# Kernel optimization log

Hardware: AMD Instinct MI355X
Metric: run time of the kernel (lower is better)

The kernel has to match this reference:

```python
import jax, jax.numpy as jnp
import numpy as np

N_NODES = 50000
N_EDGES = 800000
IN_DIM = 128
HEADS1, D1 = 4, 16   # hidden_dim // 4 = 16, concat -> 64
HID = HEADS1 * D1    # 64
OUT_DIM = 40
NEG_SLOPE = 0.2      # PyG GATConv default


def setup_inputs() -> dict:
    key = jax.random.key(0)
    ks = jax.random.split(key, 11)
    x = jax.random.normal(ks[0], (N_NODES, IN_DIM), dtype=jnp.float32)
    edge_index = jax.random.randint(ks[1], (2, N_EDGES), 0, N_NODES)
    s1 = 1.0 / np.sqrt(IN_DIM)
    s2 = 1.0 / np.sqrt(HID)
    return {
        "x": x,
        "edge_index": edge_index,
        "W1": jax.random.normal(ks[2], (IN_DIM, HEADS1 * D1), dtype=jnp.float32) * s1,
        "a_src1": jax.random.normal(ks[3], (HEADS1, D1), dtype=jnp.float32) * s2,
        "a_dst1": jax.random.normal(ks[4], (HEADS1, D1), dtype=jnp.float32) * s2,
        "b1": jnp.zeros((HID,), dtype=jnp.float32),
        "W2": jax.random.normal(ks[5], (HID, OUT_DIM), dtype=jnp.float32) * s2,
        "a_src2": jax.random.normal(ks[6], (1, OUT_DIM), dtype=jnp.float32) * s2,
        "a_dst2": jax.random.normal(ks[7], (1, OUT_DIM), dtype=jnp.float32) * s2,
        "b2": jnp.zeros((OUT_DIM,), dtype=jnp.float32),
    }


def gat_conv(x, src, dst, W, a_src, a_dst, b, heads, d, n_nodes):
    # linear projection, split into heads: [N, H, d]
    h = (x @ W).reshape(n_nodes, heads, d)
    # per-node attention logits: [N, H]
    alpha_src = jnp.einsum("nhd,hd->nh", h, a_src)
    alpha_dst = jnp.einsum("nhd,hd->nh", h, a_dst)
    # edge attention coefficients
    e = jax.nn.leaky_relu(alpha_src[src] + alpha_dst[dst], NEG_SLOPE)  # [E, H]
    # segment softmax over incoming edges of each destination node
    e_max = jax.ops.segment_max(e, dst, num_segments=n_nodes)
    e_max = jnp.where(jnp.isfinite(e_max), e_max, 0.0)
    e_exp = jnp.exp(e - e_max[dst])
    denom = jax.ops.segment_sum(e_exp, dst, num_segments=n_nodes)
    alpha = e_exp / (denom[dst] + 1e-16)  # [E, H]
    # weighted scatter-aggregate of source messages
    out = jax.ops.segment_sum(h[src] * alpha[..., None], dst, num_segments=n_nodes)
    return out.reshape(n_nodes, heads * d) + b


def reference(x, edge_index, W1, a_src1, a_dst1, b1, W2, a_src2, a_dst2, b2):
    n = x.shape[0]
    # PyG GATConv add_self_loops=True
    loop = jnp.arange(n, dtype=edge_index.dtype)
    src = jnp.concatenate([edge_index[0], loop])
    dst = jnp.concatenate([edge_index[1], loop])
    h = jax.nn.relu(gat_conv(x, src, dst, W1, a_src1, a_dst1, b1, HEADS1, D1, n))
    # dropout is identity in eval mode
    h = gat_conv(h, src, dst, W2, a_src2, a_dst2, b2, 1, OUT_DIM, n)
    return jax.nn.log_softmax(h, axis=1)
```

## Files before the change

### kernel.cpp

```cpp
#include <hip/hip_runtime.h>
#include <hip/hip_fp16.h>
#include <math.h>

#define NN    50000
#define NE0   800000
#define NE    850000
#define INDIM 128
#define HID   64
#define OUTD  40

#define NB    391
#define BSH   7
#define BCAP  3072

typedef unsigned short u16;
typedef unsigned char  u8;

__device__ inline u16 f2bf(float f) {
    unsigned u = __float_as_uint(f);
    return (u16)((u + 0x8000u) >> 16);
}
__device__ inline float bf2f(u16 h) {
    return __uint_as_float((unsigned)h << 16);
}

__global__ __launch_bounds__(512) void k_binit(int* __restrict__ bcur) {
    int i = threadIdx.x;
    if (i < NB) bcur[i] = i * BCAP;
}

__global__ __launch_bounds__(256) void k_bin(const int* __restrict__ ei,
                                             int* __restrict__ bcur,
                                             unsigned int* __restrict__ epack) {
    __shared__ int lh[NB];
    __shared__ int lbase[NB];
    __shared__ unsigned ebuf[3328];
    const int tid = threadIdx.x;
    const int CH = (NE + 255) / 256;
    const int e0 = blockIdx.x * CH;
    const int e1 = (e0 + CH < NE) ? e0 + CH : NE;
    const int cnt = e1 - e0;

    for (int i = tid; i < NB; i += 256) lh[i] = 0;
    __syncthreads();
    for (int i = tid; i < cnt; i += 256) {
        int e = e0 + i;
        int src, dst;
        if (e < NE0) { src = ei[e]; dst = ei[NE0 + e]; }
        else         { src = e - NE0; dst = src; }
        int bkt = dst >> BSH;
        ebuf[i] = (unsigned)src | ((unsigned)(dst & 127) << 16) | ((unsigned)bkt << 23);
        atomicAdd(&lh[bkt], 1);
    }
    __syncthreads();
    for (int i = tid; i < NB; i += 256) {
        int c = lh[i];
        lbase[i] = c ? atomicAdd(&bcur[i], c) : 0;
        lh[i] = 0;
    }
    __syncthreads();
    for (int i = tid; i < cnt; i += 256) {
        unsigned rec = ebuf[i];
        int bkt = rec >> 23;
        int lpos = atomicAdd(&lh[bkt], 1);
        epack[lbase[bkt] + lpos] = rec & 0x7FFFFFu;
    }
}

__global__ __launch_bounds__(256) void k_bucket_csr(
    const int* __restrict__ bcur, const unsigned int* __restrict__ epack,
    const float* __restrict__ asrc1, const float* __restrict__ adst1,
    int* __restrict__ off_s, int* __restrict__ off_e, int* __restrict__ esrc,
    u8* __restrict__ edst8, u16* __restrict__ w1u) {
    __shared__ int lh[128];
    __shared__ int lcur[128];
    __shared__ int sblk;
    __shared__ float sadst[512];
    const int tid = threadIdx.x, lane = tid & 63;
    const int b = blockIdx.x;
    const int e0 = b * BCAP;
    const int cnt = bcur[b] - e0;

    for (int i = tid; i < 512; i += 256) {
        int gi = b * 512 + i;
        sadst[i] = (gi < NN * 4) ? adst1[gi] : 0.f;
    }
    if (tid < 128) lh[tid] = 0;
    __syncthreads();
    for (int i = tid; i < cnt; i += 256)
        atomicAdd(&lh[epack[e0 + i] >> 16], 1);
    __syncthreads();

    int v = 0, incl = 0;
    if (tid < 128) {
        v = lh[tid];
        incl = v;
#pragma unroll
        for (int s = 1; s < 64; s <<= 1) {
            int t = __shfl_up(incl, s);
            if (lane >= s) incl += t;
        }
    }
    if (tid == 63) sblk = incl;
    __syncthreads();
    if (tid >= 64 && tid < 128) incl += sblk;
    if (tid < 128) {
        int ex = e0 + incl - v;
        lcur[tid] = ex;
        int gd = b * 128 + tid;
        if (gd < NN) { off_s[gd] = ex; off_e[gd] = ex + v; }
    }
    __syncthreads();

    for (int i = tid; i < cnt; i += 256) {
        unsigned int p = epack[e0 + i];
        int s  = (int)(p & 0xFFFFu);
        int dl = (int)(p >> 16);
        int pos = atomicAdd(&lcur[dl], 1);
        esrc[pos]  = s;
        edst8[pos] = (u8)dl;
        float4 av = *(const float4*)&asrc1[(size_t)s * 4];
        const float* ad = &sadst[dl * 4];
        float e0f = av.x + ad[0], e1f = av.y + ad[1];
        float e2f = av.z + ad[2], e3f = av.w + ad[3];
        e0f = (e0f > 0.f) ? e0f : 0.2f * e0f;
        e1f = (e1f > 0.f) ? e1f : 0.2f * e1f;
        e2f = (e2f > 0.f) ? e2f : 0.2f * e2f;
        e3f = (e3f > 0.f) ? e3f : 0.2f * e3f;
        unsigned lo = (unsigned)f2bf(__expf(e0f)) | ((unsigned)f2bf(__expf(e1f)) << 16);
        unsigned hi = (unsigned)f2bf(__expf(e2f)) | ((unsigned)f2bf(__expf(e3f)) << 16);
        *(uint2*)&w1u[(size_t)pos * 4] = make_uint2(lo, hi);
    }
}

__global__ __launch_bounds__(256) void k_w2(
    const int* __restrict__ bcur, const int* __restrict__ esrc,
    const u8* __restrict__ edst8, const float* __restrict__ asrc2,
    const float* __restrict__ adst2, u16* __restrict__ w2u) {
    __shared__ float sadst[128];
    const int tid = threadIdx.x;
    const int b = blockIdx.x;
    const int e0 = b * BCAP, e1 = bcur[b];
    if (tid < 128) {
        int gd = b * 128 + tid;
        sadst[tid] = (gd < NN) ? adst2[gd] : 0.f;
    }
    __syncthreads();
    for (int i = e0 + tid; i < e1; i += 256) {
        int s = esrc[i];
        float e = asrc2[s] + sadst[edst8[i]];
        e = (e > 0.f) ? e : 0.2f * e;
        w2u[i] = f2bf(__expf(e));
    }
}

__global__ __launch_bounds__(256, 2) void k_gemm1(
    const float* __restrict__ x, const float* __restrict__ W1,
    const float* __restrict__ a_s, const float* __restrict__ a_d,
    __half* __restrict__ h1h, float* __restrict__ asrc1, float* __restrict__ adst1)
{
    __shared__ float Wl[INDIM * HID];
    __shared__ float xs[64 * 132];
    const int tid = threadIdx.x;
    const int r0 = blockIdx.x * 64;

    const float4* W4 = (const float4*)W1;
    float4* Wl4 = (float4*)Wl;
#pragma unroll
    for (int i = 0; i < 8; ++i) Wl4[tid + i * 256] = W4[tid + i * 256];

    const float4* x4 = (const float4*)x;
#pragma unroll
    for (int i = 0; i < 8; ++i) {
        int idx = tid + i * 256;
        int row = idx >> 5;
        int k4  = idx & 31;
        int nr = r0 + row;
        float4 v = make_float4(0.f, 0.f, 0.f, 0.f);
        if (nr < NN) v = x4[(size_t)nr * 32 + k4];
        *(float4*)&xs[row * 132 + k4 * 4] = v;
    }
    __syncthreads();

    const int rg = tid >> 4;
    const int cg = tid & 15;
    const int c4 = cg * 4;
    const float as0 = a_s[c4], as1v = a_s[c4+1], as2v = a_s[c4+2], as3v = a_s[c4+3];
    const float ad0 = a_d[c4], ad1v = a_d[c4+1], ad2v = a_d[c4+2], ad3v = a_d[c4+3];

    float acc[4][4];
#pragma unroll
    for (int i = 0; i < 4; ++i)
#pragma unroll
        for (int j = 0; j < 4; ++j) acc[i][j] = 0.f;

#pragma unroll 4
    for (int k4 = 0; k4 < 32; ++k4) {
        float4 xv[4];
#pragma unroll
        for (int i = 0; i < 4; ++i)
            xv[i] = *(const float4*)&xs[(rg * 4 + i) * 132 + k4 * 4];
        const float* wp = &Wl[(k4 * 4) * HID + c4];
        float4 w0 = *(const float4*)(wp);
        float4 w1 = *(const float4*)(wp + HID);
        float4 w2 = *(const float4*)(wp + 2 * HID);
        float4 w3 = *(const float4*)(wp + 3 * HID);
#pragma unroll
        for (int i = 0; i < 4; ++i) {
            acc[i][0] += xv[i].x * w0.x + xv[i].y * w1.x + xv[i].z * w2.x + xv[i].w * w3.x;
            acc[i][1] += xv[i].x * w0.y + xv[i].y * w1.y + xv[i].z * w2.y + xv[i].w * w3.y;
            acc[i][2] += xv[i].x * w0.z + xv[i].y * w1.z + xv[i].z * w2.z + xv[i].w * w3.z;
            acc[i][3] += xv[i].x * w0.w + xv[i].y * w1.w + xv[i].z * w2.w + xv[i].w * w3.w;
        }
    }

#pragma unroll
    for (int i = 0; i < 4; ++i) {
        const int n = r0 + rg * 4 + i;
        if (n < NN) {
            __half2 ha = __floats2half2_rn(acc[i][0], acc[i][1]);
            __half2 hb = __floats2half2_rn(acc[i][2], acc[i][3]);
            *(__half2*)&h1h[(size_t)n * HID + c4]     = ha;
            *(__half2*)&h1h[(size_t)n * HID + c4 + 2] = hb;
        }
        float ps = acc[i][0] * as0 + acc[i][1] * as1v + acc[i][2] * as2v + acc[i][3] * as3v;
        float pd = acc[i][0] * ad0 + acc[i][1] * ad1v + acc[i][2] * ad2v + acc[i][3] * ad3v;
        ps += __shfl_xor(ps, 1); ps += __shfl_xor(ps, 2);
        pd += __shfl_xor(pd, 1); pd += __shfl_xor(pd, 2);
        if ((cg & 3) == 0 && n < NN) {
            int head = cg >> 2;
            asrc1[n * 4 + head] = ps;
            adst1[n * 4 + head] = pd;
        }
    }
}

__global__ __launch_bounds__(256) void k_fagg1(
    const int* __restrict__ off_s, const int* __restrict__ off_e,
    const int* __restrict__ esrc, const u16* __restrict__ w1u,
    const __half* __restrict__ h1h, const float* __restrict__ b1,
    __half* __restrict__ hmid)
{
    const int wv = threadIdx.x >> 6, lane = threadIdx.x & 63;
    const int g = lane >> 4, li = lane & 15;
    const int n = blockIdx.x * 16 + wv * 4 + g;
    const int s0 = off_s[n], s1 = off_e[n];
    const int hp = li >> 2;
    const int last = s1 - 1;

    float l = 0.f, a0 = 0.f, a1 = 0.f, a2 = 0.f, a3 = 0.f;
    const char* hb = (const char*)h1h;
    for (int t = s0; t < s1; t += 8) {
        int   sx[8];
        float wx[8];
#pragma unroll
        for (int j = 0; j < 8; ++j) {
            int ix  = t + j;
            int ixc = (ix < s1) ? ix : last;
            sx[j] = esrc[ixc];
            float w = bf2f(w1u[(size_t)ixc * 4 + hp]);
            wx[j] = (ix < s1) ? w : 0.f;
        }
        float2 f0[8], f1[8];
#pragma unroll
        for (int j = 0; j < 8; ++j) {
            uint2 raw = *(const uint2*)(hb + ((size_t)sx[j] * 128 + li * 8));
            f0[j] = __half22float2(*(__half2*)&raw.x);
            f1[j] = __half22float2(*(__half2*)&raw.y);
        }
#pragma unroll
        for (int j = 0; j < 8; ++j) {
            l  += wx[j];
            a0 += wx[j] * f0[j].x;
            a1 += wx[j] * f0[j].y;
            a2 += wx[j] * f1[j].x;
            a3 += wx[j] * f1[j].y;
        }
    }
    float rcp = 1.f / l;
    float4 bv = *(const float4*)&b1[li * 4];
    float o0 = fmaxf(a0 * rcp + bv.x, 0.f);
    float o1 = fmaxf(a1 * rcp + bv.y, 0.f);
    float o2 = fmaxf(a2 * rcp + bv.z, 0.f);
    float o3 = fmaxf(a3 * rcp + bv.w, 0.f);
    __half2 ha = __floats2half2_rn(o0, o1);
    __half2 hc = __floats2half2_rn(o2, o3);
    uint2 st;
    st.x = *(unsigned*)&ha;
    st.y = *(unsigned*)&hc;
    *(uint2*)((char*)hmid + ((size_t)n * 128 + li * 8)) = st;
}

__global__ __launch_bounds__(320) void k_gemm2(
    const __half* __restrict__ hin, const float* __restrict__ W2,
    const float* __restrict__ a_s, const float* __restrict__ a_d,
    __half* __restrict__ h2h, float* __restrict__ asrc2, float* __restrict__ adst2)
{
    __shared__ float Wl[HID * OUTD];
    __shared__ float xs[32 * 68];
    __shared__ float s_as[32], s_ad[32];
    const int tid = threadIdx.x;
    const int r0 = blockIdx.x * 32;

    const float4* W4 = (const float4*)W2;
    float4* Wl4 = (float4*)Wl;
    for (int i = tid; i < 640; i += 320) Wl4[i] = W4[i];
    const uint2* x4 = (const uint2*)hin;
    for (int i = tid; i < 512; i += 320) {
        int row = i >> 4;
        int c   = i & 15;
        int nr = r0 + row;
        float4 v = make_float4(0.f, 0.f, 0.f, 0.f);
        if (nr < NN) {
            uint2 raw = x4[(size_t)nr * 16 + c];
            float2 p0 = __half22float2(*(__half2*)&raw.x);
            float2 p1 = __half22float2(*(__half2*)&raw.y);
            v = make_float4(p0.x, p0.y, p1.x, p1.y);
        }
        *(float4*)&xs[row * 68 + c * 4] = v;
    }
    if (tid < 32) { s_as[tid] = 0.f; s_ad[tid] = 0.f; }
    __syncthreads();

    const int r  = tid / 10;
    const int cg = tid % 10;
    const int c4 = cg * 4;
    float a0 = 0.f, a1 = 0.f, a2 = 0.f, a3 = 0.f;
#pragma unroll 4
    for (int k4 = 0; k4 < 16; ++k4) {
        float4 xv = *(const float4*)&xs[r * 68 + k4 * 4];
        const float* wp = &Wl[(k4 * 4) * OUTD + c4];
        float4 w0 = *(const float4*)(wp);
        float4 w1 = *(const float4*)(wp + OUTD);
        float4 w2 = *(const float4*)(wp + 2 * OUTD);
        float4 w3 = *(const float4*)(wp + 3 * OUTD);
        a0 += xv.x * w0.x + xv.y * w1.x + xv.z * w2.x + xv.w * w3.x;
        a1 += xv.x * w0.y + xv.y * w1.y + xv.z * w2.y + xv.w * w3.y;
        a2 += xv.x * w0.z + xv.y * w1.z + xv.z * w2.z + xv.w * w3.z;
        a3 += xv.x * w0.w + xv.y * w1.w + xv.z * w2.w + xv.w * w3.w;
    }
    const int n = r0 + r;
    float ps = a0 * a_s[c4] + a1 * a_s[c4 + 1] + a2 * a_s[c4 + 2] + a3 * a_s[c4 + 3];
    float pd = a0 * a_d[c4] + a1 * a_d[c4 + 1] + a2 * a_d[c4 + 2] + a3 * a_d[c4 + 3];
    atomicAdd(&s_as[r], ps);
    atomicAdd(&s_ad[r], pd);
    if (n < NN) {
        __half2 ha = __floats2half2_rn(a0, a1);
        __half2 hb = __floats2half2_rn(a2, a3);
        *(__half2*)&h2h[(size_t)n * OUTD + c4]     = ha;
        *(__half2*)&h2h[(size_t)n * OUTD + c4 + 2] = hb;
    }
    __syncthreads();
    if (tid < 32) {
        int n2 = r0 + tid;
        if (n2 < NN) { asrc2[n2] = s_as[tid]; adst2[n2] = s_ad[tid]; }
    }
}

__global__ __launch_bounds__(256) void k_fagg2(
    const int* __restrict__ off_s, const int* __restrict__ off_e,
    const int* __restrict__ esrc, const u16* __restrict__ w2u,
    const __half* __restrict__ h2h, const float* __restrict__ b2,
    float* __restrict__ out)
{
    __shared__ float svals[24][OUTD];
    const int wv = threadIdx.x >> 6, lane = threadIdx.x & 63;
    const int g = lane / 10;
    const int li = lane - g * 10;
    const bool ga = (g < 6);
    const int n = blockIdx.x * 24 + wv * 6 + (ga ? g : 0);
    const bool valid = ga && (n < NN);
    const int s0 = valid ? off_s[n] : 0;
    const int s1 = valid ? off_e[n] : 0;
    const int last = s1 - 1;

    float l = 0.f, a0 = 0.f, a1 = 0.f, a2 = 0.f, a3 = 0.f;
    const char* hb = (const char*)h2h;
    for (int t = s0; t < s1; t += 8) {
        int   sx[8];
        float wx[8];
#pragma unroll
        for (int j = 0; j < 8; ++j) {
            int ix  = t + j;
            int ixc = (ix < s1) ? ix : last;
            sx[j] = esrc[ixc];
            float w = bf2f(w2u[ixc]);
            wx[j] = (ix < s1) ? w : 0.f;
        }
        float2 f0[8], f1[8];
#pragma unroll
        for (int j = 0; j < 8; ++j) {
            uint2 raw = *(const uint2*)(hb + ((size_t)sx[j] * 80 + li * 8));
            f0[j] = __half22float2(*(__half2*)&raw.x);
            f1[j] = __half22float2(*(__half2*)&raw.y);
        }
#pragma unroll
        for (int j = 0; j < 8; ++j) {
            l  += wx[j];
            a0 += wx[j] * f0[j].x;
            a1 += wx[j] * f0[j].y;
            a2 += wx[j] * f1[j].x;
            a3 += wx[j] * f1[j].y;
        }
    }
    if (valid) {
        float rcp = 1.f / l;
        float4 bv = *(const float4*)&b2[li * 4];
        int r = wv * 6 + g;
        svals[r][li * 4]     = a0 * rcp + bv.x;
        svals[r][li * 4 + 1] = a1 * rcp + bv.y;
        svals[r][li * 4 + 2] = a2 * rcp + bv.z;
        svals[r][li * 4 + 3] = a3 * rcp + bv.w;
    }
    __syncthreads();

    for (int r = wv; r < 24; r += 4) {
        int n2 = blockIdx.x * 24 + r;
        if (n2 >= NN) continue;
        float v = (lane < OUTD) ? svals[r][lane] : -1e30f;
        float mx = v;
#pragma unroll
        for (int o = 32; o; o >>= 1) mx = fmaxf(mx, __shfl_xor(mx, o));
        float ex = (lane < OUTD) ? __expf(v - mx) : 0.f;
        float sm = ex;
#pragma unroll
        for (int o = 32; o; o >>= 1) sm += __shfl_xor(sm, o);
        if (lane < OUTD) out[(size_t)n2 * OUTD + lane] = v - mx - __logf(sm);
    }
}

extern "C" void kernel_launch(void* const* d_in, const int* in_sizes, int n_in,
                              void* d_out, int out_size, void* d_ws, size_t ws_size,
                              hipStream_t stream)
{
    const float* x   = (const float*)d_in[0];
    const int*   ei  = (const int*)  d_in[1];
    const float* W1  = (const float*)d_in[2];
    const float* as1 = (const float*)d_in[3];
    const float* ad1 = (const float*)d_in[4];
    const float* b1  = (const float*)d_in[5];
    const float* W2  = (const float*)d_in[6];
    const float* as2 = (const float*)d_in[7];
    const float* ad2 = (const float*)d_in[8];
    const float* b2  = (const float*)d_in[9];
    float* out = (float*)d_out;

    char* ws = (char*)d_ws;
    __half* h1h   = (__half*)(ws);
    __half* hmidh = (__half*)(ws +  6400000);
    __half* h2h   = (__half*)(ws + 12800000);
    float*  asrc1 = (float*) (ws + 16800000);
    float*  adst1 = (float*) (ws + 17600000);
    float*  asrc2 = (float*) (ws + 18400000);
    float*  adst2 = (float*) (ws + 18600000);
    int*    off_s = (int*)   (ws + 18800000);
    int*    off_e = (int*)   (ws + 19000000);
    unsigned int* epack = (unsigned int*)(ws + 19200000);
    int*    esrc  = (int*)   (ws + 24004608);
    u8*     edst8 = (u8*)    (ws + 28809216);
    u16*    w1u   = (u16*)   (ws + 30010368);
    u16*    w2u   = (u16*)   (ws + 39619584);
    int*    bcur  = (int*)   (ws + 42021888);

    hipLaunchKernelGGL(k_binit,      dim3(1),    dim3(512), 0, stream, bcur);
    hipLaunchKernelGGL(k_bin,        dim3(256),  dim3(256), 0, stream, ei, bcur, epack);
    hipLaunchKernelGGL(k_gemm1,      dim3(782),  dim3(256), 0, stream, x, W1, as1, ad1, h1h, asrc1, adst1);
    hipLaunchKernelGGL(k_bucket_csr, dim3(NB),   dim3(256), 0, stream, bcur, epack, asrc1, adst1, off_s, off_e, esrc, edst8, w1u);
    hipLaunchKernelGGL(k_fagg1,      dim3(3125), dim3(256), 0, stream, off_s, off_e, esrc, w1u, h1h, b1, hmidh);
    hipLaunchKernelGGL(k_gemm2,      dim3(1563), dim3(320), 0, stream, hmidh, W2, as2, ad2, h2h, asrc2, adst2);
    hipLaunchKernelGGL(k_w2,         dim3(NB),   dim3(256), 0, stream, bcur, esrc, edst8, asrc2, adst2, w2u);
    hipLaunchKernelGGL(k_fagg2,      dim3(2084), dim3(256), 0, stream, off_s, off_e, esrc, w2u, h2h, b2, out);
}
```

Before: 208.0 us.

## Compute edge attention weights inline in aggregation kernels, drop precomputed weight arrays

Edge attention weights are no longer precomputed and stored as bf16 arrays in the CSR build and in a separate k_w2 kernel. Each aggregation kernel now gathers asrc per source node and recomputes leaky-relu plus exp on the fly. The bucket-offset init is folded into block 0 of gemm1, and the launch order is changed, which removes two kernel launches and the w1u, w2u and edst8 traffic. The cost is an extra random gather of asrc and redundant exp work per edge in the aggregation loops.

```diff
diff --git a/kernel.cpp b/kernel.cpp
--- a/kernel.cpp
+++ b/kernel.cpp
@@ -14,20 +14,6 @@
 #define BCAP  3072
 
 typedef unsigned short u16;
-typedef unsigned char  u8;
-
-__device__ inline u16 f2bf(float f) {
-    unsigned u = __float_as_uint(f);
-    return (u16)((u + 0x8000u) >> 16);
-}
-__device__ inline float bf2f(u16 h) {
-    return __uint_as_float((unsigned)h << 16);
-}
-
-__global__ __launch_bounds__(512) void k_binit(int* __restrict__ bcur) {
-    int i = threadIdx.x;
-    if (i < NB) bcur[i] = i * BCAP;
-}
 
 __global__ __launch_bounds__(256) void k_bin(const int* __restrict__ ei,
                                              int* __restrict__ bcur,
@@ -69,22 +55,15 @@
 
 __global__ __launch_bounds__(256) void k_bucket_csr(
     const int* __restrict__ bcur, const unsigned int* __restrict__ epack,
-    const float* __restrict__ asrc1, const float* __restrict__ adst1,
-    int* __restrict__ off_s, int* __restrict__ off_e, int* __restrict__ esrc,
-    u8* __restrict__ edst8, u16* __restrict__ w1u) {
+    int* __restrict__ off_s, int* __restrict__ off_e, int* __restrict__ esrc) {
     __shared__ int lh[128];
     __shared__ int lcur[128];
     __shared__ int sblk;
-    __shared__ float sadst[512];
     const int tid = threadIdx.x, lane = tid & 63;
     const int b = blockIdx.x;
     const int e0 = b * BCAP;
     const int cnt = bcur[b] - e0;
 
-    for (int i = tid; i < 512; i += 256) {
-        int gi = b * 512 + i;
-        sadst[i] = (gi < NN * 4) ? adst1[gi] : 0.f;
-    }
     if (tid < 128) lh[tid] = 0;
     __syncthreads();
     for (int i = tid; i < cnt; i += 256)
@@ -114,55 +93,25 @@
 
     for (int i = tid; i < cnt; i += 256) {
         unsigned int p = epack[e0 + i];
-        int s  = (int)(p & 0xFFFFu);
-        int dl = (int)(p >> 16);
-        int pos = atomicAdd(&lcur[dl], 1);
-        esrc[pos]  = s;
-        edst8[pos] = (u8)dl;
-        float4 av = *(const float4*)&asrc1[(size_t)s * 4];
-        const float* ad = &sadst[dl * 4];
-        float e0f = av.x + ad[0], e1f = av.y + ad[1];
-        float e2f = av.z + ad[2], e3f = av.w + ad[3];
-        e0f = (e0f > 0.f) ? e0f : 0.2f * e0f;
-        e1f = (e1f > 0.f) ? e1f : 0.2f * e1f;
-        e2f = (e2f > 0.f) ? e2f : 0.2f * e2f;
-        e3f = (e3f > 0.f) ? e3f : 0.2f * e3f;
-        unsigned lo = (unsigned)f2bf(__expf(e0f)) | ((unsigned)f2bf(__expf(e1f)) << 16);
-        unsigned hi = (unsigned)f2bf(__expf(e2f)) | ((unsigned)f2bf(__expf(e3f)) << 16);
-        *(uint2*)&w1u[(size_t)pos * 4] = make_uint2(lo, hi);
-    }
-}
-
-__global__ __launch_bounds__(256) void k_w2(
-    const int* __restrict__ bcur, const int* __restrict__ esrc,
-    const u8* __restrict__ edst8, const float* __restrict__ asrc2,
-    const float* __restrict__ adst2, u16* __restrict__ w2u) {
-    __shared__ float sadst[128];
-    const int tid = threadIdx.x;
-    const int b = blockIdx.x;
-    const int e0 = b * BCAP, e1 = bcur[b];
-    if (tid < 128) {
-        int gd = b * 128 + tid;
-        sadst[tid] = (gd < NN) ? adst2[gd] : 0.f;
-    }
-    __syncthreads();
-    for (int i = e0 + tid; i < e1; i += 256) {
-        int s = esrc[i];
-        float e = asrc2[s] + sadst[edst8[i]];
-        e = (e > 0.f) ? e : 0.2f * e;
-        w2u[i] = f2bf(__expf(e));
+        int pos = atomicAdd(&lcur[p >> 16], 1);
+        esrc[pos] = (int)(p & 0xFFFFu);
     }
 }
 
 __global__ __launch_bounds__(256, 2) void k_gemm1(
     const float* __restrict__ x, const float* __restrict__ W1,
     const float* __restrict__ a_s, const float* __restrict__ a_d,
-    __half* __restrict__ h1h, float* __restrict__ asrc1, float* __restrict__ adst1)
+    __half* __restrict__ h1h, float* __restrict__ asrc1, float* __restrict__ adst1,
+    int* __restrict__ bcur)
 {
     __shared__ float Wl[INDIM * HID];
     __shared__ float xs[64 * 132];
     const int tid = threadIdx.x;
     const int r0 = blockIdx.x * 64;
+
+    if (blockIdx.x == 0) {
+        for (int i = tid; i < NB; i += 256) bcur[i] = i * BCAP;
+    }
 
     const float4* W4 = (const float4*)W1;
     float4* Wl4 = (float4*)Wl;
@@ -237,7 +186,8 @@
 
 __global__ __launch_bounds__(256) void k_fagg1(
     const int* __restrict__ off_s, const int* __restrict__ off_e,
-    const int* __restrict__ esrc, const u16* __restrict__ w1u,
+    const int* __restrict__ esrc, const float* __restrict__ asrc1,
+    const float* __restrict__ adst1,
     const __half* __restrict__ h1h, const float* __restrict__ b1,
     __half* __restrict__ hmid)
 {
@@ -246,21 +196,24 @@
     const int n = blockIdx.x * 16 + wv * 4 + g;
     const int s0 = off_s[n], s1 = off_e[n];
     const int hp = li >> 2;
+    const float adst = adst1[n * 4 + hp];
     const int last = s1 - 1;
 
     float l = 0.f, a0 = 0.f, a1 = 0.f, a2 = 0.f, a3 = 0.f;
     const char* hb = (const char*)h1h;
     for (int t = s0; t < s1; t += 8) {
-        int   sx[8];
-        float wx[8];
+        int sx[8];
+        int ok[8];
 #pragma unroll
         for (int j = 0; j < 8; ++j) {
             int ix  = t + j;
-            int ixc = (ix < s1) ? ix : last;
+            ok[j] = (ix < s1);
+            int ixc = ok[j] ? ix : last;
             sx[j] = esrc[ixc];
-            float w = bf2f(w1u[(size_t)ixc * 4 + hp]);
-            wx[j] = (ix < s1) ? w : 0.f;
-        }
+        }
+        float ax[8];
+#pragma unroll
+        for (int j = 0; j < 8; ++j) ax[j] = asrc1[sx[j] * 4 + hp];
         float2 f0[8], f1[8];
 #pragma unroll
         for (int j = 0; j < 8; ++j) {
@@ -270,11 +223,15 @@
         }
 #pragma unroll
         for (int j = 0; j < 8; ++j) {
-            l  += wx[j];
-            a0 += wx[j] * f0[j].x;
-            a1 += wx[j] * f0[j].y;
-            a2 += wx[j] * f1[j].x;
-            a3 += wx[j] * f1[j].y;
+            float e = ax[j] + adst;
+            e = (e > 0.f) ? e : 0.2f * e;
+            float w = __expf(e);
+            w = ok[j] ? w : 0.f;
+            l  += w;
+            a0 += w * f0[j].x;
+            a1 += w * f0[j].y;
+            a2 += w * f1[j].x;
+            a3 += w * f1[j].y;
         }
     }
     float rcp = 1.f / l;
@@ -359,7 +316,8 @@
 
 __global__ __launch_bounds__(256) void k_fagg2(
     const int* __restrict__ off_s, const int* __restrict__ off_e,
-    const int* __restrict__ esrc, const u16* __restrict__ w2u,
+    const int* __restrict__ esrc, const float* __restrict__ asrc2,
+    const float* __restrict__ adst2,
     const __half* __restrict__ h2h, const float* __restrict__ b2,
     float* __restrict__ out)
 {
@@ -372,21 +330,24 @@
     const bool valid = ga && (n < NN);
     const int s0 = valid ? off_s[n] : 0;
     const int s1 = valid ? off_e[n] : 0;
+    const float adst = valid ? adst2[n] : 0.f;
     const int last = s1 - 1;
 
     float l = 0.f, a0 = 0.f, a1 = 0.f, a2 = 0.f, a3 = 0.f;
     const char* hb = (const char*)h2h;
     for (int t = s0; t < s1; t += 8) {
-        int   sx[8];
-        float wx[8];
+        int sx[8];
+        int ok[8];
 #pragma unroll
         for (int j = 0; j < 8; ++j) {
             int ix  = t + j;
-            int ixc = (ix < s1) ? ix : last;
+            ok[j] = (ix < s1);
+            int ixc = ok[j] ? ix : last;
             sx[j] = esrc[ixc];
-            float w = bf2f(w2u[ixc]);
-            wx[j] = (ix < s1) ? w : 0.f;
-        }
+        }
+        float ax[8];
+#pragma unroll
+        for (int j = 0; j < 8; ++j) ax[j] = asrc2[sx[j]];
         float2 f0[8], f1[8];
 #pragma unroll
         for (int j = 0; j < 8; ++j) {
@@ -396,11 +357,15 @@
         }
 #pragma unroll
         for (int j = 0; j < 8; ++j) {
-            l  += wx[j];
-            a0 += wx[j] * f0[j].x;
-            a1 += wx[j] * f0[j].y;
-            a2 += wx[j] * f1[j].x;
-            a3 += wx[j] * f1[j].y;
+            float e = ax[j] + adst;
+            e = (e > 0.f) ? e : 0.2f * e;
+            float w = __expf(e);
+            w = ok[j] ? w : 0.f;
+            l  += w;
+            a0 += w * f0[j].x;
+            a1 += w * f0[j].y;
+            a2 += w * f1[j].x;
+            a3 += w * f1[j].y;
         }
     }
     if (valid) {
@@ -457,17 +422,12 @@
     int*    off_e = (int*)   (ws + 19000000);
     unsigned int* epack = (unsigned int*)(ws + 19200000);
     int*    esrc  = (int*)   (ws + 24004608);
-    u8*     edst8 = (u8*)    (ws + 28809216);
-    u16*    w1u   = (u16*)   (ws + 30010368);
-    u16*    w2u   = (u16*)   (ws + 39619584);
-    int*    bcur  = (int*)   (ws + 42021888);
-
-    hipLaunchKernelGGL(k_binit,      dim3(1),    dim3(512), 0, stream, bcur);
+    int*    bcur  = (int*)   (ws + 28809216);
+
+    hipLaunchKernelGGL(k_gemm1,      dim3(782),  dim3(256), 0, stream, x, W1, as1, ad1, h1h, asrc1, adst1, bcur);
     hipLaunchKernelGGL(k_bin,        dim3(256),  dim3(256), 0, stream, ei, bcur, epack);
-    hipLaunchKernelGGL(k_gemm1,      dim3(782),  dim3(256), 0, stream, x, W1, as1, ad1, h1h, asrc1, adst1);
-    hipLaunchKernelGGL(k_bucket_csr, dim3(NB),   dim3(256), 0, stream, bcur, epack, asrc1, adst1, off_s, off_e, esrc, edst8, w1u);
-    hipLaunchKernelGGL(k_fagg1,      dim3(3125), dim3(256), 0, stream, off_s, off_e, esrc, w1u, h1h, b1, hmidh);
+    hipLaunchKernelGGL(k_bucket_csr, dim3(NB),   dim3(256), 0, stream, bcur, epack, off_s, off_e, esrc);
+    hipLaunchKernelGGL(k_fagg1,      dim3(3125), dim3(256), 0, stream, off_s, off_e, esrc, asrc1, adst1, h1h, b1, hmidh);
     hipLaunchKernelGGL(k_gemm2,      dim3(1563), dim3(320), 0, stream, hmidh, W2, as2, ad2, h2h, asrc2, adst2);
-    hipLaunchKernelGGL(k_w2,         dim3(NB),   dim3(256), 0, stream, bcur, esrc, edst8, asrc2, adst2, w2u);
-    hipLaunchKernelGGL(k_fagg2,      dim3(2084), dim3(256), 0, stream, off_s, off_e, esrc, w2u, h2h, b2, out);
-}
+    hipLaunchKernelGGL(k_fagg2,      dim3(2084), dim3(256), 0, stream, off_s, off_e, esrc, asrc2, adst2, h2h, b2, out);
+}
```

Measured after the change: 192.3 us (median of 2 runs). 1.08x faster.
